# Optimization experiments

Measured on AMD Instinct MI355X. Metric: run time of the kernel, lower is better.

Reference implementation:

```python
import jax, jax.numpy as jnp
import numpy as np

EMB, HEADS = 1024, 16
HD = EMB // HEADS


def setup_inputs() -> dict:
    key = jax.random.key(0)
    ks = jax.random.split(key, 9)
    B, T, C = 4, 2048, EMB
    s = 1.0 / np.sqrt(C)
    return {
        "x": jax.random.normal(ks[0], (B, T, C), jnp.float32),
        "Wq": jax.random.normal(ks[1], (C, C), jnp.float32) * s,
        "bq": jnp.zeros((C,), jnp.float32),
        "Wk": jax.random.normal(ks[2], (C, C), jnp.float32) * s,
        "bk": jnp.zeros((C,), jnp.float32),
        "Wv": jax.random.normal(ks[3], (C, C), jnp.float32) * s,
        "bv": jnp.zeros((C,), jnp.float32),
        "Wo": jax.random.normal(ks[4], (C, C), jnp.float32) * s,
        "bo": jnp.zeros((C,), jnp.float32),
    }


def _attn(x, Wq, bq, Wk, bk, Wv, bv, Wo, bo):
    B, T, C = x.shape
    # [B,T,C] -> [B,H,T,hd]
    def split(h):
        return h.reshape(B, T, HEADS, HD).transpose(0, 2, 1, 3)
    q = split(x @ Wq + bq)
    k = split(x @ Wk + bk)
    v = split(x @ Wv + bv)
    att = jnp.einsum("bhtd,bhsd->bhts", q, k) * (1.0 / np.sqrt(HD))
    causal = jnp.tril(jnp.ones((T, T), bool))  # [T,T]
    att = jnp.where(causal, att, -jnp.inf)
    att = jax.nn.softmax(att, axis=-1)
    y = jnp.einsum("bhts,bhsd->bhtd", att, v)
    y = y.transpose(0, 2, 1, 3).reshape(B, T, C)
    return y @ Wo + bo


def reference(x, Wq, bq, Wk, bk, Wv, bv, Wo, bo):
    return _attn(x, Wq, bq, Wk, bk, Wv, bv, Wo, bo)
```

## Files before the change

kernel.cpp:

```cpp
#include <hip/hip_runtime.h>
#include <cmath>

#define EMB 1024
#define HEADS 16
#define HD 64
#define BATCH 4
#define SEQ 2048
#define MTOT (BATCH * SEQ)

typedef __attribute__((ext_vector_type(8))) short short8;
typedef __attribute__((ext_vector_type(4))) float f32x4;
typedef __attribute__((ext_vector_type(16))) float f32x16;

__device__ __forceinline__ float b2f(unsigned short u) {
  union { unsigned int i; float f; } c; c.i = ((unsigned int)u) << 16; return c.f;
}
__device__ __forceinline__ unsigned short f2b(float f) {
  union { float f; unsigned int i; } c; c.f = f;
  unsigned int x = c.i;
  return (unsigned short)((x + 0x7fffu + ((x >> 16) & 1u)) >> 16);
}

#define GLD16(gp, lp) __builtin_amdgcn_global_load_lds( \
    (__attribute__((address_space(1))) unsigned int*)(gp), \
    (__attribute__((address_space(3))) unsigned int*)(lp), 16, 0, 0)

__global__ __launch_bounds__(256) void prep(
    const float* __restrict__ x, unsigned short* __restrict__ xb,
    const float* __restrict__ W0, const float* __restrict__ W1,
    const float* __restrict__ W2, const float* __restrict__ W3,
    unsigned short* __restrict__ Wt) {
  const int b = blockIdx.x;
  if (b < 4096) {
    const size_t i = ((size_t)b * 256 + threadIdx.x) * 8;
    const float4 a = *(const float4*)(x + i);
    const float4 c = *(const float4*)(x + i + 4);
    ushort4 lo = {f2b(a.x), f2b(a.y), f2b(a.z), f2b(a.w)};
    ushort4 hi = {f2b(c.x), f2b(c.y), f2b(c.z), f2b(c.w)};
    *(ushort4*)(xb + i) = lo;
    *(ushort4*)(xb + i + 4) = hi;
  } else {
    __shared__ float T[32][33];
    const int bb = b - 4096;
    const int z = bb >> 10;
    const float* W = (z == 0) ? W0 : (z == 1) ? W1 : (z == 2) ? W2 : W3;
    unsigned short* out = Wt + (size_t)z * EMB * EMB;
    const int k0 = (bb & 31) * 32, n0 = ((bb >> 5) & 31) * 32;
    const int tx = threadIdx.x & 31, ty = threadIdx.x >> 5;
#pragma unroll
    for (int r = 0; r < 4; ++r)
      T[ty + r * 8][tx] = W[(size_t)(k0 + ty + r * 8) * EMB + n0 + tx];
    __syncthreads();
#pragma unroll
    for (int r = 0; r < 4; ++r)
      out[(size_t)(n0 + ty + r * 8) * EMB + k0 + tx] = f2b(T[tx][ty + r * 8]);
  }
}

#define GEMM_STAGE64(Asrc_, Bsrc_, kb_)                                     \
  do {                                                                      \
    _Pragma("unroll")                                                       \
    for (int j_ = 0; j_ < 4; ++j_) {                                        \
      const int t_ = w * 4 + j_;                                            \
      const int r_ = t_ * 8 + r8;                                           \
      GLD16((Asrc_) + (size_t)(row0 + r_) * EMB + (kb_) + c8x,              \
            &As[t_ * 512]);                                                 \
      GLD16((Bsrc_) + (size_t)(col0 + r_) * EMB + (kb_) + c8x,              \
            &Bs[t_ * 512]);                                                 \
    }                                                                       \
  } while (0)

#define GEMM_KLOOP64(Asrc_, Bsrc_)                                          \
  const int r8 = lane >> 3;                                                 \
  const int c8x = ((lane & 7) ^ r8) * 8;                                    \
  for (int kb = 0; kb < EMB; kb += 64) {                                    \
    if (kb) __syncthreads();                                                \
    GEMM_STAGE64(Asrc_, Bsrc_, kb);                                         \
    __syncthreads();                                                        \
    _Pragma("unroll")                                                       \
    for (int kc = 0; kc < 2; ++kc) {                                        \
      short8 af[4], bf[4];                                                  \
      _Pragma("unroll")                                                     \
      for (int i = 0; i < 4; ++i)                                           \
        af[i] = *(const short8*)                                            \
            &As[(wm + i * 16 + m) * 64 + (((kc * 4 + g) ^ (m & 7)) * 8)];   \
      _Pragma("unroll")                                                     \
      for (int j = 0; j < 4; ++j)                                           \
        bf[j] = *(const short8*)                                            \
            &Bs[(wn + j * 16 + m) * 64 + (((kc * 4 + g) ^ (m & 7)) * 8)];   \
      _Pragma("unroll")                                                     \
      for (int i = 0; i < 4; ++i)                                           \
        _Pragma("unroll")                                                   \
        for (int j = 0; j < 4; ++j)                                         \
          acc[i][j] = __builtin_amdgcn_mfma_f32_16x16x32_bf16(              \
              af[i], bf[j], acc[i][j], 0, 0, 0);                            \
    }                                                                       \
  }

template <int OUTMODE>
__global__ __launch_bounds__(256) void gemm_mfma(
    const unsigned short* __restrict__ A, const unsigned short* __restrict__ Bt,
    const float* __restrict__ bias, void* __restrict__ outp) {
  __shared__ unsigned short As[128 * 64];
  __shared__ unsigned short Bs[128 * 64];
  const int tid = threadIdx.x;
  const int w = tid >> 6, lane = tid & 63;
  const int g = lane >> 4, m = lane & 15;
  const int row0 = blockIdx.x * 128, col0 = blockIdx.y * 128;
  const int wm = (w >> 1) * 64, wn = (w & 1) * 64;

  f32x4 acc[4][4];
#pragma unroll
  for (int i = 0; i < 4; ++i)
#pragma unroll
    for (int j = 0; j < 4; ++j) acc[i][j] = (f32x4){0.f, 0.f, 0.f, 0.f};

  GEMM_KLOOP64(A, Bt)

  float bv[4];
#pragma unroll
  for (int j = 0; j < 4; ++j) bv[j] = bias[col0 + wn + j * 16 + m];

#pragma unroll
  for (int i = 0; i < 4; ++i)
#pragma unroll
    for (int j = 0; j < 4; ++j)
#pragma unroll
      for (int r = 0; r < 4; ++r) {
        const size_t row = row0 + wm + i * 16 + g * 4 + r;
        const size_t col = col0 + wn + j * 16 + m;
        const float val = acc[i][j][r] + bv[j];
        if constexpr (OUTMODE == 0) ((float*)outp)[row * EMB + col] = val;
        else ((unsigned short*)outp)[row * EMB + col] = f2b(val);
      }
}

__global__ __launch_bounds__(256) void gemm_qkv(
    const unsigned short* __restrict__ A, const unsigned short* __restrict__ Wt,
    const float* __restrict__ b0, const float* __restrict__ b1,
    const float* __restrict__ b2, unsigned short* __restrict__ out) {
  __shared__ unsigned short As[128 * 64];
  __shared__ unsigned short Bs[128 * 64];
  const int z = blockIdx.z;
  const unsigned short* Bt = Wt + (size_t)z * EMB * EMB;
  const float* bias = (z == 0) ? b0 : ((z == 1) ? b1 : b2);
  const int tid = threadIdx.x;
  const int w = tid >> 6, lane = tid & 63;
  const int g = lane >> 4, m = lane & 15;
  const int row0 = blockIdx.x * 128, col0 = blockIdx.y * 128;
  const int wm = (w >> 1) * 64, wn = (w & 1) * 64;

  f32x4 acc[4][4];
#pragma unroll
  for (int i = 0; i < 4; ++i)
#pragma unroll
    for (int j = 0; j < 4; ++j) acc[i][j] = (f32x4){0.f, 0.f, 0.f, 0.f};

  GEMM_KLOOP64(A, Bt)

  float bv[4];
#pragma unroll
  for (int j = 0; j < 4; ++j) bv[j] = bias[col0 + wn + j * 16 + m];

  if (z == 2) {
    unsigned short* Vt = out + (size_t)2 * MTOT * EMB;
    const int bi = row0 >> 11;
    const int tb = (row0 & 2047) + wm;
#pragma unroll
    for (int i = 0; i < 4; ++i)
#pragma unroll
      for (int j = 0; j < 4; ++j) {
        const int col = col0 + wn + j * 16 + m;
        const int t0 = tb + i * 16 + g * 4;
        ushort4 pv = {f2b(acc[i][j][0] + bv[j]), f2b(acc[i][j][1] + bv[j]),
                      f2b(acc[i][j][2] + bv[j]), f2b(acc[i][j][3] + bv[j])};
        *(ushort4*)&Vt[(size_t)(bi * 1024 + col) * SEQ + t0] = pv;
      }
  } else {
    unsigned short* O = out + (size_t)z * MTOT * EMB;
#pragma unroll
    for (int i = 0; i < 4; ++i)
#pragma unroll
      for (int j = 0; j < 4; ++j)
#pragma unroll
        for (int r = 0; r < 4; ++r) {
          const size_t row = row0 + wm + i * 16 + g * 4 + r;
          const size_t col = col0 + wn + j * 16 + m;
          O[row * EMB + col] = f2b(acc[i][j][r] + bv[j]);
        }
  }
}

__global__ __launch_bounds__(256, 4) void flash_mfma(
    const unsigned short* __restrict__ Qg, const unsigned short* __restrict__ Kg,
    const unsigned short* __restrict__ Vtg, unsigned short* __restrict__ Yg) {
  __shared__ unsigned short Kl[2][64 * 64];
  __shared__ unsigned short Vl[2][64 * 64];
  const int tid = threadIdx.x;
  const int w = tid >> 6, lane = tid & 63;
  const int ql = lane & 31;
  const int hi = lane >> 5;

  const int gid = blockIdx.x;
  const int g2 = gid & 3;
  const int hb = (gid >> 2) & 63;
  const int g8 = gid >> 8;
  const int q4 = g2 * 4 + g8;
  const int qb = (q4 & 1) ? (q4 >> 1) : (15 - (q4 >> 1));
  const int bi = hb >> 4, hd = hb & 15;

  const size_t base = ((size_t)bi * SEQ) * EMB + (size_t)hd * HD;
  const size_t vtrow0 = (size_t)(bi * HEADS + hd) * HD;

  const int r8 = lane >> 3;
  const int c8 = ((lane & 7) ^ r8) * 8;

#define STAGE(tile_, buf_)                                                  \
  do {                                                                      \
    const int s0_ = (tile_) * 64;                                           \
    _Pragma("unroll")                                                       \
    for (int L = 0; L < 2; ++L) {                                           \
      const int rb_ = 16 * w + 8 * L;                                       \
      GLD16(Kg + base + (size_t)(s0_ + rb_ + r8) * EMB + c8,                \
            &Kl[buf_][rb_ * 64]);                                           \
    }                                                                       \
    _Pragma("unroll")                                                       \
    for (int L = 0; L < 2; ++L) {                                           \
      const int rb_ = 16 * w + 8 * L;                                       \
      GLD16(Vtg + (vtrow0 + rb_ + r8) * SEQ + s0_ + c8,                     \
            &Vl[buf_][rb_ * 64]);                                           \
    }                                                                       \
  } while (0)

  const int q0w = qb * 128 + 32 * w;
  const int q = q0w + ql;

  short8 qf[4];
#pragma unroll
  for (int s = 0; s < 4; ++s) {
    const uint4 u = *(const uint4*)(
        Qg + base + (size_t)q * EMB + s * 16 + hi * 8);
    const unsigned short* t = (const unsigned short*)&u;
    short8 qv;
#pragma unroll
    for (int j = 0; j < 8; ++j) qv[j] = (short)f2b(b2f(t[j]) * 0.18033688f);
    qf[s] = qv;
  }

  f32x16 acc[2];
#pragma unroll
  for (int db = 0; db < 2; ++db)
#pragma unroll
    for (int i = 0; i < 16; ++i) acc[db][i] = 0.f;
  float m_r = -INFINITY, l_r = 0.f;

  const int nt = 2 * qb + 2;
  STAGE(0, 0);

  int buf = 0;
  for (int t = 0; t < nt; ++t) {
    asm volatile("s_waitcnt vmcnt(0)" ::: "memory");
    __builtin_amdgcn_s_barrier();
    if (t + 1 < nt) STAGE(t + 1, buf ^ 1);
    const int s0 = t * 64;
    if (s0 <= q0w + 31) {
      const unsigned short* K0 = Kl[buf];
      const unsigned short* V0 = Vl[buf];

      f32x16 sA[2];
      __builtin_amdgcn_s_setprio(1);
#pragma unroll
      for (int n = 0; n < 2; ++n) {
        const int row = 32 * n + ql;
        const int rb = row * 64, rk = row & 7;
        f32x16 z;
#pragma unroll
        for (int i = 0; i < 16; ++i) z[i] = 0.f;
#pragma unroll
        for (int s = 0; s < 4; ++s) {
          const short8 kf =
              *(const short8*)&K0[rb + (((2 * s + hi) ^ rk) * 8)];
          z = __builtin_amdgcn_mfma_f32_32x32x16_bf16(kf, qf[s], z, 0, 0, 0);
        }
        sA[n] = z;
      }
      __builtin_amdgcn_s_setprio(0);

      if (s0 + 63 > q) {
#pragma unroll
        for (int n = 0; n < 2; ++n)
#pragma unroll
          for (int r = 0; r < 16; ++r)
            if (s0 + 32 * n + (r & 3) + 8 * (r >> 2) + 4 * hi > q)
              sA[n][r] = -INFINITY;
      }

      float m8[8];
#pragma unroll
      for (int i = 0; i < 8; ++i)
        m8[i] = fmaxf(fmaxf(sA[0][2 * i], sA[0][2 * i + 1]),
                      fmaxf(sA[1][2 * i], sA[1][2 * i + 1]));
      float tmax = fmaxf(fmaxf(fmaxf(m8[0], m8[1]), fmaxf(m8[2], m8[3])),
                         fmaxf(fmaxf(m8[4], m8[5]), fmaxf(m8[6], m8[7])));
      tmax = fmaxf(tmax, __shfl_xor(tmax, 32));

      if (!__all(tmax - m_r <= 11.f)) {
        const float nm = fmaxf(m_r, tmax);
        float sc;
        const float d0 = m_r - nm;
        asm("v_exp_f32 %0, %1" : "=v"(sc) : "v"(d0));
#pragma unroll
        for (int db = 0; db < 2; ++db)
#pragma unroll
          for (int i = 0; i < 16; ++i) acc[db][i] *= sc;
        l_r *= sc;
        m_r = nm;
      }

#pragma unroll
      for (int n = 0; n < 2; ++n)
#pragma unroll
        for (int r = 0; r < 16; ++r) {
          float p;
          const float d1 = sA[n][r] - m_r;
          asm("v_exp_f32 %0, %1" : "=v"(p) : "v"(d1));
          sA[n][r] = p;
        }
      float s8[8];
#pragma unroll
      for (int i = 0; i < 8; ++i)
        s8[i] = (sA[0][2 * i] + sA[0][2 * i + 1]) +
                (sA[1][2 * i] + sA[1][2 * i + 1]);
      float ps = ((s8[0] + s8[1]) + (s8[2] + s8[3])) +
                 ((s8[4] + s8[5]) + (s8[6] + s8[7]));
      ps += __shfl_xor(ps, 32);
      l_r += ps;

      unsigned int pk[2][8];
#pragma unroll
      for (int n = 0; n < 2; ++n)
#pragma unroll
        for (int i = 0; i < 8; ++i) {
          unsigned int d;
          asm("v_cvt_pk_bf16_f32 %0, %1, %2"
              : "=v"(d) : "v"(sA[n][2 * i]), "v"(sA[n][2 * i + 1]));
          pk[n][i] = d;
        }
      union { unsigned int u[4]; short8 s; } pf[4];
#pragma unroll
      for (int ks = 0; ks < 4; ++ks) {
        const int n = ks >> 1, k4 = (ks & 1) * 4;
        unsigned int a0 = pk[n][k4 + 0], a1 = pk[n][k4 + 1];
        unsigned int b0 = pk[n][k4 + 2], b1 = pk[n][k4 + 3];
        asm("v_permlane32_swap_b32 %0, %1" : "+v"(a0), "+v"(b0));
        asm("v_permlane32_swap_b32 %0, %1" : "+v"(a1), "+v"(b1));
        pf[ks].u[0] = a0; pf[ks].u[1] = a1;
        pf[ks].u[2] = b0; pf[ks].u[3] = b1;
      }

      __builtin_amdgcn_s_setprio(1);
#pragma unroll
      for (int db = 0; db < 2; ++db) {
        const int row = 32 * db + ql;
        const int rb = row * 64, rk = row & 7;
#pragma unroll
        for (int ks = 0; ks < 4; ++ks) {
          const short8 vf =
              *(const short8*)&V0[rb + (((2 * ks + hi) ^ rk) * 8)];
          acc[db] = __builtin_amdgcn_mfma_f32_32x32x16_bf16(vf, pf[ks].s,
                                                            acc[db], 0, 0, 0);
        }
      }
      __builtin_amdgcn_s_setprio(0);
    }
    buf ^= 1;
  }

  const float iv = 1.f / l_r;
  unsigned short* Yrow = Yg + base + (size_t)q * EMB;
#pragma unroll
  for (int db = 0; db < 2; ++db)
#pragma unroll
    for (int r = 0; r < 16; r += 2) {
      unsigned int d;
      const float lo = acc[db][r] * iv, hh = acc[db][r + 1] * iv;
      asm("v_cvt_pk_bf16_f32 %0, %1, %2" : "=v"(d) : "v"(lo), "v"(hh));
      const int col = 32 * db + (r & 3) + 8 * (r >> 2) + 4 * hi;
      *(unsigned int*)(Yrow + col) = d;
    }
#undef STAGE
}

extern "C" void kernel_launch(void* const* d_in, const int* in_sizes, int n_in,
                              void* d_out, int out_size, void* d_ws, size_t ws_size,
                              hipStream_t stream) {
  const float* x  = (const float*)d_in[0];
  const float* Wq = (const float*)d_in[1];
  const float* bq = (const float*)d_in[2];
  const float* Wk = (const float*)d_in[3];
  const float* bk = (const float*)d_in[4];
  const float* Wv = (const float*)d_in[5];
  const float* bv = (const float*)d_in[6];
  const float* Wo = (const float*)d_in[7];
  const float* bo = (const float*)d_in[8];
  float* out = (float*)d_out;

  unsigned short* wqt = (unsigned short*)d_ws;
  unsigned short* wot = wqt + (size_t)3 * EMB * EMB;
  unsigned short* Q  = wqt + (size_t)4 * EMB * EMB;
  unsigned short* K  = Q + (size_t)MTOT * EMB;
  unsigned short* Vt = K + (size_t)MTOT * EMB;
  unsigned short* Y  = Vt + (size_t)MTOT * EMB;
  unsigned short* xb = Y + (size_t)MTOT * EMB;

  prep<<<dim3(8192), 256, 0, stream>>>(x, xb, Wq, Wk, Wv, Wo, wqt);

  gemm_qkv<<<dim3(MTOT / 128, EMB / 128, 3), 256, 0, stream>>>(
      xb, wqt, bq, bk, bv, Q);
  flash_mfma<<<dim3(1024), 256, 0, stream>>>(Q, K, Vt, Y);
  gemm_mfma<0><<<dim3(MTOT / 128, EMB / 128), 256, 0, stream>>>(
      Y, wot, bo, out);
}
```

Measured before the change: 150.1 us.

## Split flash attention KV loop across two wave groups and merge partial softmax

The attention kernel now runs 512 threads per block. Two groups of four waves each process alternating 64-key tiles, with their own double-buffered K/V shared memory. At the end, group 1 writes its partial accumulators and (max, sum) into shared memory, and group 0 combines them with a log-sum-exp rescale before writing the output. The aim is to halve the serial KV loop length per block and hide latency. In exchange it doubles shared memory per block and adds a final merge with extra barriers. The block-to-tile mapping is also simplified to plain heavy-first ordering, dropping the previous interleave.

New measurement: 150.7 us. About the same (+0.4%).

```diff
diff --git a/kernel.cpp b/kernel.cpp
--- a/kernel.cpp
+++ b/kernel.cpp
@@ -191,23 +191,24 @@
   }
 }
 
-__global__ __launch_bounds__(256, 4) void flash_mfma(
+__global__ __launch_bounds__(512, 4) void flash_mfma(
     const unsigned short* __restrict__ Qg, const unsigned short* __restrict__ Kg,
     const unsigned short* __restrict__ Vtg, unsigned short* __restrict__ Yg) {
-  __shared__ unsigned short Kl[2][64 * 64];
-  __shared__ unsigned short Vl[2][64 * 64];
+  __shared__ unsigned short Kl[2][2][64 * 64];
+  __shared__ unsigned short Vl[2][2][64 * 64];
+  __shared__ float ml[4][32][2];
   const int tid = threadIdx.x;
-  const int w = tid >> 6, lane = tid & 63;
+  const int wv = tid >> 6;
+  const int grp = wv >> 2;
+  const int w = wv & 3;
+  const int lane = tid & 63;
   const int ql = lane & 31;
   const int hi = lane >> 5;
 
   const int gid = blockIdx.x;
-  const int g2 = gid & 3;
-  const int hb = (gid >> 2) & 63;
-  const int g8 = gid >> 8;
-  const int q4 = g2 * 4 + g8;
-  const int qb = (q4 & 1) ? (q4 >> 1) : (15 - (q4 >> 1));
-  const int bi = hb >> 4, hd = hb & 15;
+  const int qb = 15 - (gid >> 6);
+  const int bh = gid & 63;
+  const int bi = bh >> 4, hd = bh & 15;
 
   const size_t base = ((size_t)bi * SEQ) * EMB + (size_t)hd * HD;
   const size_t vtrow0 = (size_t)(bi * HEADS + hd) * HD;
@@ -222,13 +223,13 @@
     for (int L = 0; L < 2; ++L) {                                           \
       const int rb_ = 16 * w + 8 * L;                                       \
       GLD16(Kg + base + (size_t)(s0_ + rb_ + r8) * EMB + c8,                \
-            &Kl[buf_][rb_ * 64]);                                           \
+            &Kl[grp][buf_][rb_ * 64]);                                      \
     }                                                                       \
     _Pragma("unroll")                                                       \
     for (int L = 0; L < 2; ++L) {                                           \
       const int rb_ = 16 * w + 8 * L;                                       \
       GLD16(Vtg + (vtrow0 + rb_ + r8) * SEQ + s0_ + c8,                     \
-            &Vl[buf_][rb_ * 64]);                                           \
+            &Vl[grp][buf_][rb_ * 64]);                                      \
     }                                                                       \
   } while (0)
 
@@ -254,18 +255,18 @@
     for (int i = 0; i < 16; ++i) acc[db][i] = 0.f;
   float m_r = -INFINITY, l_r = 0.f;
 
-  const int nt = 2 * qb + 2;
-  STAGE(0, 0);
+  const int ntg = qb + 1;
+  STAGE(grp, 0);
 
   int buf = 0;
-  for (int t = 0; t < nt; ++t) {
+  for (int s = 0; s < ntg; ++s) {
     asm volatile("s_waitcnt vmcnt(0)" ::: "memory");
     __builtin_amdgcn_s_barrier();
-    if (t + 1 < nt) STAGE(t + 1, buf ^ 1);
-    const int s0 = t * 64;
+    if (s + 1 < ntg) STAGE(2 * (s + 1) + grp, buf ^ 1);
+    const int s0 = (2 * s + grp) * 64;
     if (s0 <= q0w + 31) {
-      const unsigned short* K0 = Kl[buf];
-      const unsigned short* V0 = Vl[buf];
+      const unsigned short* K0 = Kl[grp][buf];
+      const unsigned short* V0 = Vl[grp][buf];
 
       f32x16 sA[2];
       __builtin_amdgcn_s_setprio(1);
@@ -277,10 +278,10 @@
 #pragma unroll
         for (int i = 0; i < 16; ++i) z[i] = 0.f;
 #pragma unroll
-        for (int s = 0; s < 4; ++s) {
+        for (int s2 = 0; s2 < 4; ++s2) {
           const short8 kf =
-              *(const short8*)&K0[rb + (((2 * s + hi) ^ rk) * 8)];
-          z = __builtin_amdgcn_mfma_f32_32x32x16_bf16(kf, qf[s], z, 0, 0, 0);
+              *(const short8*)&K0[rb + (((2 * s2 + hi) ^ rk) * 8)];
+          z = __builtin_amdgcn_mfma_f32_32x32x16_bf16(kf, qf[s2], z, 0, 0, 0);
         }
         sA[n] = z;
       }
@@ -376,18 +377,42 @@
     buf ^= 1;
   }
 
-  const float iv = 1.f / l_r;
-  unsigned short* Yrow = Yg + base + (size_t)q * EMB;
-#pragma unroll
-  for (int db = 0; db < 2; ++db)
-#pragma unroll
-    for (int r = 0; r < 16; r += 2) {
-      unsigned int d;
-      const float lo = acc[db][r] * iv, hh = acc[db][r + 1] * iv;
-      asm("v_cvt_pk_bf16_f32 %0, %1, %2" : "=v"(d) : "v"(lo), "v"(hh));
-      const int col = 32 * db + (r & 3) + 8 * (r >> 2) + 4 * hi;
-      *(unsigned int*)(Yrow + col) = d;
-    }
+  __builtin_amdgcn_s_barrier();
+  float* mb = (float*)Kl;
+  const int mbase = (wv & 3) * 64 * 32 + lane * 32;
+  if (grp == 1) {
+#pragma unroll
+    for (int db = 0; db < 2; ++db)
+#pragma unroll
+      for (int i = 0; i < 16; ++i)
+        mb[mbase + ((db * 16 + i) ^ (lane & 31))] = acc[db][i];
+    if (hi == 0) { ml[w][ql][0] = m_r; ml[w][ql][1] = l_r; }
+  }
+  __builtin_amdgcn_s_barrier();
+  if (grp == 0) {
+    const float mB = ml[w][ql][0], lB = ml[w][ql][1];
+    const float nm = fmaxf(m_r, mB);
+    float eA, eB;
+    const float dA = m_r - nm, dB = mB - nm;
+    asm("v_exp_f32 %0, %1" : "=v"(eA) : "v"(dA));
+    asm("v_exp_f32 %0, %1" : "=v"(eB) : "v"(dB));
+    const float l = l_r * eA + lB * eB;
+    const float iv = 1.f / l;
+    unsigned short* Yrow = Yg + base + (size_t)q * EMB;
+#pragma unroll
+    for (int db = 0; db < 2; ++db)
+#pragma unroll
+      for (int r = 0; r < 16; r += 2) {
+        const float oB0 = mb[mbase + ((db * 16 + r) ^ (lane & 31))];
+        const float oB1 = mb[mbase + ((db * 16 + r + 1) ^ (lane & 31))];
+        const float lo = (acc[db][r] * eA + oB0 * eB) * iv;
+        const float hh = (acc[db][r + 1] * eA + oB1 * eB) * iv;
+        unsigned int d;
+        asm("v_cvt_pk_bf16_f32 %0, %1, %2" : "=v"(d) : "v"(lo), "v"(hh));
+        const int col = 32 * db + (r & 3) + 8 * (r >> 2) + 4 * hi;
+        *(unsigned int*)(Yrow + col) = d;
+      }
+  }
 #undef STAGE
 }
 
@@ -417,7 +442,7 @@
 
   gemm_qkv<<<dim3(MTOT / 128, EMB / 128, 3), 256, 0, stream>>>(
       xb, wqt, bq, bk, bv, Q);
-  flash_mfma<<<dim3(1024), 256, 0, stream>>>(Q, K, Vt, Y);
+  flash_mfma<<<dim3(1024), 512, 0, stream>>>(Q, K, Vt, Y);
   gemm_mfma<0><<<dim3(MTOT / 128, EMB / 128), 256, 0, stream>>>(
       Y, wot, bo, out);
 }
```

## Process two 32-row query sub-tiles per wave to reuse K/V LDS fragments

Applied to the files above, without the earlier changes.

Each wave now handles 64 query rows (two 32-row sub-tiles), so each block covers 256 queries and the grid halves to 512 blocks. Each K and V fragment read from LDS feeds two MFMAs, which halves LDS traffic and global K/V staging per query. Occupancy drops (launch bounds 4→2 blocks per CU) because registers roughly double. The block-to-tile ordering also changes to a simpler pairing of heavy and light causal tiles, with only 512 blocks to balance across the CUs.

After: 164.2 us. 9.4% more time.

```diff
diff --git a/kernel.cpp b/kernel.cpp
--- a/kernel.cpp
+++ b/kernel.cpp
@@ -191,7 +191,7 @@
   }
 }
 
-__global__ __launch_bounds__(256, 4) void flash_mfma(
+__global__ __launch_bounds__(256, 2) void flash_mfma(
     const unsigned short* __restrict__ Qg, const unsigned short* __restrict__ Kg,
     const unsigned short* __restrict__ Vtg, unsigned short* __restrict__ Yg) {
   __shared__ unsigned short Kl[2][64 * 64];
@@ -202,12 +202,10 @@
   const int hi = lane >> 5;
 
   const int gid = blockIdx.x;
-  const int g2 = gid & 3;
-  const int hb = (gid >> 2) & 63;
-  const int g8 = gid >> 8;
-  const int q4 = g2 * 4 + g8;
-  const int qb = (q4 & 1) ? (q4 >> 1) : (15 - (q4 >> 1));
-  const int bi = hb >> 4, hd = hb & 15;
+  const int idx = gid >> 6;
+  const int qb = (idx < 4) ? 7 - idx : idx - 4;
+  const int bh = gid & 63;
+  const int bi = bh >> 4, hd = bh & 15;
 
   const size_t base = ((size_t)bi * SEQ) * EMB + (size_t)hd * HD;
   const size_t vtrow0 = (size_t)(bi * HEADS + hd) * HD;
@@ -232,29 +230,32 @@
     }                                                                       \
   } while (0)
 
-  const int q0w = qb * 128 + 32 * w;
-  const int q = q0w + ql;
-
-  short8 qf[4];
-#pragma unroll
-  for (int s = 0; s < 4; ++s) {
-    const uint4 u = *(const uint4*)(
-        Qg + base + (size_t)q * EMB + s * 16 + hi * 8);
-    const unsigned short* t = (const unsigned short*)&u;
-    short8 qv;
-#pragma unroll
-    for (int j = 0; j < 8; ++j) qv[j] = (short)f2b(b2f(t[j]) * 0.18033688f);
-    qf[s] = qv;
-  }
-
-  f32x16 acc[2];
-#pragma unroll
-  for (int db = 0; db < 2; ++db)
-#pragma unroll
-    for (int i = 0; i < 16; ++i) acc[db][i] = 0.f;
-  float m_r = -INFINITY, l_r = 0.f;
-
-  const int nt = 2 * qb + 2;
+  const int q0w = qb * 256 + 64 * w;
+
+  short8 qf[2][4];
+#pragma unroll
+  for (int q2 = 0; q2 < 2; ++q2)
+#pragma unroll
+    for (int s = 0; s < 4; ++s) {
+      const uint4 u = *(const uint4*)(
+          Qg + base + (size_t)(q0w + 32 * q2 + ql) * EMB + s * 16 + hi * 8);
+      const unsigned short* t = (const unsigned short*)&u;
+      short8 qv;
+#pragma unroll
+      for (int j = 0; j < 8; ++j) qv[j] = (short)f2b(b2f(t[j]) * 0.18033688f);
+      qf[q2][s] = qv;
+    }
+
+  f32x16 acc[2][2];
+#pragma unroll
+  for (int q2 = 0; q2 < 2; ++q2)
+#pragma unroll
+    for (int db = 0; db < 2; ++db)
+#pragma unroll
+      for (int i = 0; i < 16; ++i) acc[q2][db][i] = 0.f;
+  float m_r[2] = {-INFINITY, -INFINITY}, l_r[2] = {0.f, 0.f};
+
+  const int nt = 4 * qb + 4;
   STAGE(0, 0);
 
   int buf = 0;
@@ -263,99 +264,108 @@
     __builtin_amdgcn_s_barrier();
     if (t + 1 < nt) STAGE(t + 1, buf ^ 1);
     const int s0 = t * 64;
-    if (s0 <= q0w + 31) {
+    if (s0 <= q0w + 63) {
       const unsigned short* K0 = Kl[buf];
       const unsigned short* V0 = Vl[buf];
 
-      f32x16 sA[2];
+      f32x16 sA[2][2];
       __builtin_amdgcn_s_setprio(1);
 #pragma unroll
       for (int n = 0; n < 2; ++n) {
         const int row = 32 * n + ql;
         const int rb = row * 64, rk = row & 7;
-        f32x16 z;
-#pragma unroll
-        for (int i = 0; i < 16; ++i) z[i] = 0.f;
-#pragma unroll
-        for (int s = 0; s < 4; ++s) {
+        f32x16 z0, z1;
+#pragma unroll
+        for (int i = 0; i < 16; ++i) { z0[i] = 0.f; z1[i] = 0.f; }
+#pragma unroll
+        for (int s2 = 0; s2 < 4; ++s2) {
           const short8 kf =
-              *(const short8*)&K0[rb + (((2 * s + hi) ^ rk) * 8)];
-          z = __builtin_amdgcn_mfma_f32_32x32x16_bf16(kf, qf[s], z, 0, 0, 0);
+              *(const short8*)&K0[rb + (((2 * s2 + hi) ^ rk) * 8)];
+          z0 = __builtin_amdgcn_mfma_f32_32x32x16_bf16(kf, qf[0][s2], z0,
+                                                       0, 0, 0);
+          z1 = __builtin_amdgcn_mfma_f32_32x32x16_bf16(kf, qf[1][s2], z1,
+                                                       0, 0, 0);
         }
-        sA[n] = z;
+        sA[0][n] = z0; sA[1][n] = z1;
       }
       __builtin_amdgcn_s_setprio(0);
 
-      if (s0 + 63 > q) {
-#pragma unroll
-        for (int n = 0; n < 2; ++n)
-#pragma unroll
-          for (int r = 0; r < 16; ++r)
-            if (s0 + 32 * n + (r & 3) + 8 * (r >> 2) + 4 * hi > q)
-              sA[n][r] = -INFINITY;
-      }
-
-      float m8[8];
-#pragma unroll
-      for (int i = 0; i < 8; ++i)
-        m8[i] = fmaxf(fmaxf(sA[0][2 * i], sA[0][2 * i + 1]),
-                      fmaxf(sA[1][2 * i], sA[1][2 * i + 1]));
-      float tmax = fmaxf(fmaxf(fmaxf(m8[0], m8[1]), fmaxf(m8[2], m8[3])),
-                         fmaxf(fmaxf(m8[4], m8[5]), fmaxf(m8[6], m8[7])));
-      tmax = fmaxf(tmax, __shfl_xor(tmax, 32));
-
-      if (!__all(tmax - m_r <= 11.f)) {
-        const float nm = fmaxf(m_r, tmax);
-        float sc;
-        const float d0 = m_r - nm;
-        asm("v_exp_f32 %0, %1" : "=v"(sc) : "v"(d0));
-#pragma unroll
-        for (int db = 0; db < 2; ++db)
-#pragma unroll
-          for (int i = 0; i < 16; ++i) acc[db][i] *= sc;
-        l_r *= sc;
-        m_r = nm;
-      }
-
-#pragma unroll
-      for (int n = 0; n < 2; ++n)
-#pragma unroll
-        for (int r = 0; r < 16; ++r) {
-          float p;
-          const float d1 = sA[n][r] - m_r;
-          asm("v_exp_f32 %0, %1" : "=v"(p) : "v"(d1));
-          sA[n][r] = p;
+      union { unsigned int u[4]; short8 s; } pf[2][4];
+#pragma unroll
+      for (int q2 = 0; q2 < 2; ++q2) {
+        if (s0 <= q0w + 32 * q2 + 31) {
+          const int q = q0w + 32 * q2 + ql;
+          if (s0 + 63 > q) {
+#pragma unroll
+            for (int n = 0; n < 2; ++n)
+#pragma unroll
+              for (int r = 0; r < 16; ++r)
+                if (s0 + 32 * n + (r & 3) + 8 * (r >> 2) + 4 * hi > q)
+                  sA[q2][n][r] = -INFINITY;
+          }
+
+          float m8[8];
+#pragma unroll
+          for (int i = 0; i < 8; ++i)
+            m8[i] = fmaxf(fmaxf(sA[q2][0][2 * i], sA[q2][0][2 * i + 1]),
+                          fmaxf(sA[q2][1][2 * i], sA[q2][1][2 * i + 1]));
+          float tmax = fmaxf(fmaxf(fmaxf(m8[0], m8[1]), fmaxf(m8[2], m8[3])),
+                             fmaxf(fmaxf(m8[4], m8[5]), fmaxf(m8[6], m8[7])));
+          tmax = fmaxf(tmax, __shfl_xor(tmax, 32));
+
+          if (!__all(tmax - m_r[q2] <= 11.f)) {
+            const float nm = fmaxf(m_r[q2], tmax);
+            float sc;
+            const float d0 = m_r[q2] - nm;
+            asm("v_exp_f32 %0, %1" : "=v"(sc) : "v"(d0));
+#pragma unroll
+            for (int db = 0; db < 2; ++db)
+#pragma unroll
+              for (int i = 0; i < 16; ++i) acc[q2][db][i] *= sc;
+            l_r[q2] *= sc;
+            m_r[q2] = nm;
+          }
+
+#pragma unroll
+          for (int n = 0; n < 2; ++n)
+#pragma unroll
+            for (int r = 0; r < 16; ++r) {
+              float p;
+              const float d1 = sA[q2][n][r] - m_r[q2];
+              asm("v_exp_f32 %0, %1" : "=v"(p) : "v"(d1));
+              sA[q2][n][r] = p;
+            }
+          float s8[8];
+#pragma unroll
+          for (int i = 0; i < 8; ++i)
+            s8[i] = (sA[q2][0][2 * i] + sA[q2][0][2 * i + 1]) +
+                    (sA[q2][1][2 * i] + sA[q2][1][2 * i + 1]);
+          float ps = ((s8[0] + s8[1]) + (s8[2] + s8[3])) +
+                     ((s8[4] + s8[5]) + (s8[6] + s8[7]));
+          ps += __shfl_xor(ps, 32);
+          l_r[q2] += ps;
+
+          unsigned int pk[2][8];
+#pragma unroll
+          for (int n = 0; n < 2; ++n)
+#pragma unroll
+            for (int i = 0; i < 8; ++i) {
+              unsigned int d;
+              asm("v_cvt_pk_bf16_f32 %0, %1, %2"
+                  : "=v"(d) : "v"(sA[q2][n][2 * i]), "v"(sA[q2][n][2 * i + 1]));
+              pk[n][i] = d;
+            }
+#pragma unroll
+          for (int ks = 0; ks < 4; ++ks) {
+            const int n = ks >> 1, k4 = (ks & 1) * 4;
+            unsigned int a0 = pk[n][k4 + 0], a1 = pk[n][k4 + 1];
+            unsigned int b0 = pk[n][k4 + 2], b1 = pk[n][k4 + 3];
+            asm("v_permlane32_swap_b32 %0, %1" : "+v"(a0), "+v"(b0));
+            asm("v_permlane32_swap_b32 %0, %1" : "+v"(a1), "+v"(b1));
+            pf[q2][ks].u[0] = a0; pf[q2][ks].u[1] = a1;
+            pf[q2][ks].u[2] = b0; pf[q2][ks].u[3] = b1;
+          }
         }
-      float s8[8];
-#pragma unroll
-      for (int i = 0; i < 8; ++i)
-        s8[i] = (sA[0][2 * i] + sA[0][2 * i + 1]) +
-                (sA[1][2 * i] + sA[1][2 * i + 1]);
-      float ps = ((s8[0] + s8[1]) + (s8[2] + s8[3])) +
-                 ((s8[4] + s8[5]) + (s8[6] + s8[7]));
-      ps += __shfl_xor(ps, 32);
-      l_r += ps;
-
-      unsigned int pk[2][8];
-#pragma unroll
-      for (int n = 0; n < 2; ++n)
-#pragma unroll
-        for (int i = 0; i < 8; ++i) {
-          unsigned int d;
-          asm("v_cvt_pk_bf16_f32 %0, %1, %2"
-              : "=v"(d) : "v"(sA[n][2 * i]), "v"(sA[n][2 * i + 1]));
-          pk[n][i] = d;
-        }
-      union { unsigned int u[4]; short8 s; } pf[4];
-#pragma unroll
-      for (int ks = 0; ks < 4; ++ks) {
-        const int n = ks >> 1, k4 = (ks & 1) * 4;
-        unsigned int a0 = pk[n][k4 + 0], a1 = pk[n][k4 + 1];
-        unsigned int b0 = pk[n][k4 + 2], b1 = pk[n][k4 + 3];
-        asm("v_permlane32_swap_b32 %0, %1" : "+v"(a0), "+v"(b0));
-        asm("v_permlane32_swap_b32 %0, %1" : "+v"(a1), "+v"(b1));
-        pf[ks].u[0] = a0; pf[ks].u[1] = a1;
-        pf[ks].u[2] = b0; pf[ks].u[3] = b1;
       }
 
       __builtin_amdgcn_s_setprio(1);
@@ -367,8 +377,11 @@
         for (int ks = 0; ks < 4; ++ks) {
           const short8 vf =
               *(const short8*)&V0[rb + (((2 * ks + hi) ^ rk) * 8)];
-          acc[db] = __builtin_amdgcn_mfma_f32_32x32x16_bf16(vf, pf[ks].s,
-                                                            acc[db], 0, 0, 0);
+#pragma unroll
+          for (int q2 = 0; q2 < 2; ++q2)
+            if (s0 <= q0w + 32 * q2 + 31)
+              acc[q2][db] = __builtin_amdgcn_mfma_f32_32x32x16_bf16(
+                  vf, pf[q2][ks].s, acc[q2][db], 0, 0, 0);
         }
       }
       __builtin_amdgcn_s_setprio(0);
@@ -376,18 +389,21 @@
     buf ^= 1;
   }
 
-  const float iv = 1.f / l_r;
-  unsigned short* Yrow = Yg + base + (size_t)q * EMB;
-#pragma unroll
-  for (int db = 0; db < 2; ++db)
-#pragma unroll
-    for (int r = 0; r < 16; r += 2) {
-      unsigned int d;
-      const float lo = acc[db][r] * iv, hh = acc[db][r + 1] * iv;
-      asm("v_cvt_pk_bf16_f32 %0, %1, %2" : "=v"(d) : "v"(lo), "v"(hh));
-      const int col = 32 * db + (r & 3) + 8 * (r >> 2) + 4 * hi;
-      *(unsigned int*)(Yrow + col) = d;
-    }
+#pragma unroll
+  for (int q2 = 0; q2 < 2; ++q2) {
+    const float iv = 1.f / l_r[q2];
+    unsigned short* Yrow = Yg + base + (size_t)(q0w + 32 * q2 + ql) * EMB;
+#pragma unroll
+    for (int db = 0; db < 2; ++db)
+#pragma unroll
+      for (int r = 0; r < 16; r += 2) {
+        unsigned int d;
+        const float lo = acc[q2][db][r] * iv, hh = acc[q2][db][r + 1] * iv;
+        asm("v_cvt_pk_bf16_f32 %0, %1, %2" : "=v"(d) : "v"(lo), "v"(hh));
+        const int col = 32 * db + (r & 3) + 8 * (r >> 2) + 4 * hi;
+        *(unsigned int*)(Yrow + col) = d;
+      }
+  }
 #undef STAGE
 }
 
@@ -417,7 +433,7 @@
 
   gemm_qkv<<<dim3(MTOT / 128, EMB / 128, 3), 256, 0, stream>>>(
       xb, wqt, bq, bk, bv, Q);
-  flash_mfma<<<dim3(1024), 256, 0, stream>>>(Q, K, Vt, Y);
+  flash_mfma<<<dim3(512), 256, 0, stream>>>(Q, K, Vt, Y);
   gemm_mfma<0><<<dim3(MTOT / 128, EMB / 128), 256, 0, stream>>>(
       Y, wot, bo, out);
 }
```
